# Kernel optimization log

Measured on AMD Instinct MI355X. Metric: run time of the kernel, lower is better.

Reference implementation:

```python
import jax, jax.numpy as jnp
import numpy as np

B, D, H, E = 32768, 128, 512, 16

def setup_inputs() -> dict:
    key = jax.random.key(0)
    ks = jax.random.split(key, 5)
    x = jax.random.normal(ks[0], (B, 1, D), dtype=jnp.float32)
    s1 = 1.0 / float(np.sqrt(H))   # init_ uses last-dim size: w1 last dim = H
    s2 = 1.0 / float(np.sqrt(D))   # w2 last dim = D
    sg = 1.0 / float(np.sqrt(D))   # nn.Linear(D, E) default init scale
    w1 = jax.random.uniform(ks[1], (E, D, H), minval=-s1, maxval=s1, dtype=jnp.float32)
    w2 = jax.random.uniform(ks[2], (E, H, D), minval=-s2, maxval=s2, dtype=jnp.float32)
    wg = jax.random.uniform(ks[3], (D, E), minval=-sg, maxval=sg, dtype=jnp.float32)
    bg = jax.random.uniform(ks[4], (E,), minval=-sg, maxval=sg, dtype=jnp.float32)
    return {"x": x, "w1": w1, "w2": w2, "wg": wg, "bg": bg}

def reference(x, w1, w2, wg, bg):
    xt = x[:, 0, :]                                   # (B, D); seq dim is 1 by construction
    logits = xt @ wg + bg                             # (B, E)
    topk_vals, topk_idx = jax.lax.top_k(logits, 1)    # (B, 1) each
    scores = jax.nn.softmax(topk_vals, axis=-1)       # (B, 1); all ones for k=1
    # every expert processes every token (faithful to the reference)
    hidden = jax.nn.gelu(jnp.einsum('bd,edh->ebh', xt, w1), approximate=False)  # (E, B, H)
    eout = jnp.einsum('ebh,ehd->ebd', hidden, w2)     # (E, B, D)
    # gather selected expert per token, scale, sum over k
    sel = jnp.take_along_axis(eout.transpose(1, 0, 2), topk_idx[:, :, None], axis=1)  # (B, 1, D)
    return (sel * scores[:, :, None]).sum(axis=1)     # (B, D)
```

## Files before the change

### kernel.cpp

```cpp
#include <hip/hip_runtime.h>
#include <hip/hip_bf16.h>
#include <math.h>

#define NB 32768
#define DD 128
#define HH 512
#define EE 16
#define TM 64

typedef __attribute__((ext_vector_type(8))) short short8;
typedef __attribute__((ext_vector_type(4))) float f32x4;
typedef __attribute__((ext_vector_type(16))) float f32x16;

__device__ __forceinline__ unsigned short f2bf(float f) {
  union { float f; unsigned u; } v; v.f = f;
  unsigned r = v.u + 0x7fffu + ((v.u >> 16) & 1u);
  return (unsigned short)(r >> 16);
}

__device__ __forceinline__ float fast_erf(float z) {
  float a = fabsf(z);
  float t = __builtin_amdgcn_rcpf(1.0f + 0.3275911f * a);
  float y = t * (0.254829592f + t * (-0.284496736f + t * (1.421413741f +
            t * (-1.453152027f + t * 1.061405429f))));
  float r = 1.0f - y * __expf(-a * a);
  return z < 0.0f ? -r : r;
}

__global__ __launch_bounds__(256) void prep_kernel(
    const float* __restrict__ x, const float* __restrict__ wg,
    const float* __restrict__ bg, const float* __restrict__ w1,
    const float* __restrict__ w2, int* __restrict__ counts,
    int* __restrict__ rows, unsigned short* __restrict__ wP) {
  __shared__ __align__(16) char smem[50816];
  int tid = threadIdx.x;

  if (blockIdx.x >= 512) {
    int l = tid & 63, lc = l & 31, hi = l >> 5;
    int gw = (blockIdx.x - 512) * 4 + (tid >> 6);
    #pragma unroll
    for (int i = 0; i < 2; ++i) {
      int kb = gw * 2 + i;
      int e = kb >> 8, v = kb & 255;
      float vals[8];
      if (v < 128) {
        int hc = v >> 4, t = (v >> 3) & 1, ks = v & 7;
        int h = hc * 64 + t * 32 + lc;
        const float* src = w1 + (size_t)e * DD * HH + h;
        int d0 = ks * 16 + hi * 8;
        #pragma unroll
        for (int j = 0; j < 8; ++j) vals[j] = src[(size_t)(d0 + j) * HH];
      } else {
        int b2 = v - 128;
        int hc = b2 >> 4, s = (b2 >> 2) & 3, dt = b2 & 3;
        int dout = dt * 32 + lc;
        const float* src = w2 + (size_t)e * HH * DD + dout;
        #pragma unroll
        for (int j = 0; j < 8; ++j) {
          int hp = hc * 64 + (s >> 1) * 32 + (j & 3) + 8 * ((s & 1) + 2 * (j >> 2)) + 4 * hi;
          vals[j] = src[(size_t)hp * DD];
        }
      }
      ushort4 p0, p1;
      p0.x = f2bf(vals[0]); p0.y = f2bf(vals[1]); p0.z = f2bf(vals[2]); p0.w = f2bf(vals[3]);
      p1.x = f2bf(vals[4]); p1.y = f2bf(vals[5]); p1.z = f2bf(vals[6]); p1.w = f2bf(vals[7]);
      unsigned short* dst = wP + (size_t)kb * 512 + l * 8;
      *(ushort4*)dst = p0;
      *(ushort4*)(dst + 4) = p1;
    }
    return;
  }

  float  (*sx)[132] = (float (*)[132])smem;
  double (*swg)[EE] = (double (*)[EE])(smem + 33792);
  int* lcnt  = (int*)(smem + 50176);
  int* gbase = lcnt + EE;
  int* lslot = gbase + EE;
  int* lexp  = lslot + 64;

  int base = blockIdx.x * 64;
  if (tid < EE) lcnt[tid] = 0;
  for (int i = tid; i < DD * EE; i += 256) swg[i >> 4][i & 15] = (double)wg[i];
  {
    int r = tid >> 2, c0 = (tid & 3) * 32;
    const float4* src = (const float4*)(x + (size_t)(base + r) * DD + c0);
    #pragma unroll
    for (int i = 0; i < 8; ++i)
      *(float4*)&sx[r][c0 + i * 4] = src[i];
  }
  __syncthreads();

  int r = tid >> 2;
  int e0 = (tid & 3) * 4;
  double acc[4];
  #pragma unroll
  for (int j = 0; j < 4; ++j) acc[j] = (double)bg[e0 + j];

  #pragma unroll 4
  for (int d = 0; d < DD; ++d) {
    double xv = (double)sx[r][d];
    #pragma unroll
    for (int j = 0; j < 4; ++j)
      acc[j] += xv * swg[d][e0 + j];
  }

  int beste = 0; double bestv = acc[0];
  #pragma unroll
  for (int j = 1; j < 4; ++j)
    if (acc[j] > bestv) { bestv = acc[j]; beste = j; }
  int ge = e0 + beste;

  #pragma unroll
  for (int off = 1; off < 4; off <<= 1) {
    double ov = __shfl_xor(bestv, off);
    int oe = __shfl_xor(ge, off);
    if (ov > bestv || (ov == bestv && oe < ge)) { bestv = ov; ge = oe; }
  }

  if ((tid & 3) == 0) {
    lslot[r] = atomicAdd(&lcnt[ge], 1);
    lexp[r] = ge;
  }
  __syncthreads();
  if (tid < EE && lcnt[tid] > 0)
    gbase[tid] = atomicAdd(&counts[tid], lcnt[tid]);
  __syncthreads();
  if ((tid & 3) == 0) {
    int e2 = lexp[r];
    rows[e2 * NB + gbase[e2] + lslot[r]] = base + r;
  }
}

__global__ __launch_bounds__(128, 2) void moe_gemm(
    const float* __restrict__ x, const unsigned short* __restrict__ wP,
    const int* __restrict__ counts, const int* __restrict__ rows,
    float* __restrict__ out) {
  int e = blockIdx.x;
  int cnt = counts[e];
  int base = blockIdx.y * TM;
  if (base >= cnt) return;

  int tid = threadIdx.x;
  int wv = tid >> 6, l = tid & 63;
  int lc = l & 31, hi = l >> 5;
  int mb = base + wv * 32;
  if (mb >= cnt) return;

  const unsigned short* we = wP + (size_t)e * 256 * 512;

  short8 xa[8];
  {
    int ridx = mb + lc; if (ridx >= cnt) ridx = cnt - 1;
    int grow = rows[e * NB + ridx];
    const float* xr = x + (size_t)grow * DD + hi * 8;
    #pragma unroll
    for (int ks = 0; ks < 8; ++ks) {
      f32x4 v0 = *(const f32x4*)(xr + ks * 16);
      f32x4 v1 = *(const f32x4*)(xr + ks * 16 + 4);
      short8 a;
      a[0] = f2bf(v0[0]); a[1] = f2bf(v0[1]); a[2] = f2bf(v0[2]); a[3] = f2bf(v0[3]);
      a[4] = f2bf(v1[0]); a[5] = f2bf(v1[1]); a[6] = f2bf(v1[2]); a[7] = f2bf(v1[3]);
      xa[ks] = a;
    }
  }

  f32x16 acc2[4];
  #pragma unroll
  for (int dt = 0; dt < 4; ++dt)
    #pragma unroll
    for (int r = 0; r < 16; ++r) acc2[dt][r] = 0.f;

  for (int hc = 0; hc < 8; ++hc) {
    const unsigned short* wc1 = we + (size_t)hc * 16 * 512 + l * 8;
    const unsigned short* wc2 = we + (size_t)(128 + hc * 16) * 512 + l * 8;
    #pragma unroll
    for (int t = 0; t < 2; ++t) {
      f32x16 a1;
      #pragma unroll
      for (int r = 0; r < 16; ++r) a1[r] = 0.f;
      #pragma unroll
      for (int ks = 0; ks < 8; ++ks) {
        short8 wf = *(const short8*)(wc1 + (t * 8 + ks) * 512);
        a1 = __builtin_amdgcn_mfma_f32_32x32x16_bf16(wf, xa[ks], a1, 0, 0, 0);
      }
      #pragma unroll
      for (int s2 = 0; s2 < 2; ++s2) {
        short8 hf8;
        #pragma unroll
        for (int j = 0; j < 8; ++j) {
          int r = (j & 3) | (s2 << 2) | ((j >> 2) << 3);
          float v = a1[r];
          float g = 0.5f * v * (1.0f + fast_erf(v * 0.70710678118654752f));
          hf8[j] = (short)f2bf(g);
        }
        int s = 2 * t + s2;
        #pragma unroll
        for (int dt = 0; dt < 4; ++dt) {
          short8 wf = *(const short8*)(wc2 + (s * 4 + dt) * 512);
          acc2[dt] = __builtin_amdgcn_mfma_f32_32x32x16_bf16(hf8, wf, acc2[dt], 0, 0, 0);
        }
      }
    }
  }

  #pragma unroll
  for (int reg = 0; reg < 16; ++reg) {
    int m = (reg & 3) + 8 * (reg >> 2) + 4 * hi;
    int ridx = mb + m;
    if (ridx < cnt) {
      int grow = rows[e * NB + ridx];
      float* op = out + (size_t)grow * DD + lc;
      op[0]  = acc2[0][reg];
      op[32] = acc2[1][reg];
      op[64] = acc2[2][reg];
      op[96] = acc2[3][reg];
    }
  }
}

extern "C" void kernel_launch(void* const* d_in, const int* in_sizes, int n_in,
                              void* d_out, int out_size, void* d_ws, size_t ws_size,
                              hipStream_t stream) {
  const float* x  = (const float*)d_in[0];
  const float* w1 = (const float*)d_in[1];
  const float* w2 = (const float*)d_in[2];
  const float* wg = (const float*)d_in[3];
  const float* bg = (const float*)d_in[4];
  float* out = (float*)d_out;

  int* counts = (int*)d_ws;
  int* rows   = (int*)((char*)d_ws + 1024);
  unsigned short* wP = (unsigned short*)((char*)d_ws + 1024 + (size_t)EE * NB * 4);

  hipMemsetAsync(d_ws, 0, 64, stream);
  hipLaunchKernelGGL(prep_kernel, dim3(1024), dim3(256), 0, stream,
                     x, wg, bg, w1, w2, counts, rows, wP);
  hipLaunchKernelGGL(moe_gemm, dim3(EE, NB / TM), dim3(128), 0, stream,
                     x, wP, counts, rows, out);
}
```

Before: 139.7 us.

## Split MoE hidden dimension across four waves with shared-memory reduction

Each block of the MoE GEMM now handles 32 token rows with four waves. Each wave covers a quarter of the hidden dimension (two of eight H-chunks) instead of one wave covering all of H for 32 rows. The partial second-GEMM accumulators are reduced through 32 KB of LDS in two tree steps, and the final stores are split across two waves. This shortens the serial per-wave chain and raises parallelism when per-expert token counts are uneven. The cost is extra LDS traffic, three barriers, and 32 KB of shared memory per block, which may limit occupancy.

```diff
diff --git a/kernel.cpp b/kernel.cpp
--- a/kernel.cpp
+++ b/kernel.cpp
@@ -6,7 +6,7 @@
 #define DD 128
 #define HH 512
 #define EE 16
-#define TM 64
+#define TM 32
 
 typedef __attribute__((ext_vector_type(8))) short short8;
 typedef __attribute__((ext_vector_type(4))) float f32x4;
@@ -131,7 +131,7 @@
   }
 }
 
-__global__ __launch_bounds__(128, 2) void moe_gemm(
+__global__ __launch_bounds__(256, 4) void moe_gemm(
     const float* __restrict__ x, const unsigned short* __restrict__ wP,
     const int* __restrict__ counts, const int* __restrict__ rows,
     float* __restrict__ out) {
@@ -140,17 +140,17 @@
   int base = blockIdx.y * TM;
   if (base >= cnt) return;
 
+  __shared__ float sc[8192];
+
   int tid = threadIdx.x;
-  int wv = tid >> 6, l = tid & 63;
+  int hq = tid >> 6, l = tid & 63;
   int lc = l & 31, hi = l >> 5;
-  int mb = base + wv * 32;
-  if (mb >= cnt) return;
 
   const unsigned short* we = wP + (size_t)e * 256 * 512;
 
   short8 xa[8];
   {
-    int ridx = mb + lc; if (ridx >= cnt) ridx = cnt - 1;
+    int ridx = base + lc; if (ridx >= cnt) ridx = cnt - 1;
     int grow = rows[e * NB + ridx];
     const float* xr = x + (size_t)grow * DD + hi * 8;
     #pragma unroll
@@ -170,7 +170,9 @@
     #pragma unroll
     for (int r = 0; r < 16; ++r) acc2[dt][r] = 0.f;
 
-  for (int hc = 0; hc < 8; ++hc) {
+  #pragma unroll
+  for (int hcL = 0; hcL < 2; ++hcL) {
+    int hc = hq * 2 + hcL;
     const unsigned short* wc1 = we + (size_t)hc * 16 * 512 + l * 8;
     const unsigned short* wc2 = we + (size_t)(128 + hc * 16) * 512 + l * 8;
     #pragma unroll
@@ -203,17 +205,52 @@
     }
   }
 
-  #pragma unroll
-  for (int reg = 0; reg < 16; ++reg) {
-    int m = (reg & 3) + 8 * (reg >> 2) + 4 * hi;
-    int ridx = mb + m;
-    if (ridx < cnt) {
-      int grow = rows[e * NB + ridx];
-      float* op = out + (size_t)grow * DD + lc;
-      op[0]  = acc2[0][reg];
-      op[32] = acc2[1][reg];
-      op[64] = acc2[2][reg];
-      op[96] = acc2[3][reg];
+  if (hq & 1) {
+    float* d = sc + (hq >> 1) * 4096;
+    #pragma unroll
+    for (int dt = 0; dt < 4; ++dt)
+      #pragma unroll
+      for (int r = 0; r < 16; ++r) d[(dt * 16 + r) * 64 + l] = acc2[dt][r];
+  }
+  __syncthreads();
+  if (!(hq & 1)) {
+    const float* s = sc + (hq >> 1) * 4096;
+    #pragma unroll
+    for (int dt = 0; dt < 4; ++dt)
+      #pragma unroll
+      for (int r = 0; r < 16; ++r) acc2[dt][r] += s[(dt * 16 + r) * 64 + l];
+  }
+  __syncthreads();
+  if (hq == 0) {
+    #pragma unroll
+    for (int dt = 2; dt < 4; ++dt)
+      #pragma unroll
+      for (int r = 0; r < 16; ++r) sc[((dt - 2) * 16 + r) * 64 + l] = acc2[dt][r];
+  }
+  if (hq == 2) {
+    #pragma unroll
+    for (int dt = 0; dt < 2; ++dt)
+      #pragma unroll
+      for (int r = 0; r < 16; ++r) sc[4096 + (dt * 16 + r) * 64 + l] = acc2[dt][r];
+  }
+  __syncthreads();
+  if (hq == 0 || hq == 2) {
+    int dt0 = (hq == 0) ? 0 : 2;
+    const float* s = (hq == 0) ? (sc + 4096) : sc;
+    #pragma unroll
+    for (int dd2 = 0; dd2 < 2; ++dd2)
+      #pragma unroll
+      for (int r = 0; r < 16; ++r) acc2[dt0 + dd2][r] += s[(dd2 * 16 + r) * 64 + l];
+    #pragma unroll
+    for (int reg = 0; reg < 16; ++reg) {
+      int m = (reg & 3) + 8 * (reg >> 2) + 4 * hi;
+      int ridx = base + m;
+      if (ridx < cnt) {
+        int grow = rows[e * NB + ridx];
+        float* op = out + (size_t)grow * DD + dt0 * 32 + lc;
+        op[0]  = acc2[dt0][reg];
+        op[32] = acc2[dt0 + 1][reg];
+      }
     }
   }
 }
@@ -235,6 +272,6 @@
   hipMemsetAsync(d_ws, 0, 64, stream);
   hipLaunchKernelGGL(prep_kernel, dim3(1024), dim3(256), 0, stream,
                      x, wg, bg, w1, w2, counts, rows, wP);
-  hipLaunchKernelGGL(moe_gemm, dim3(EE, NB / TM), dim3(128), 0, stream,
+  hipLaunchKernelGGL(moe_gemm, dim3(EE, NB / TM), dim3(256), 0, stream,
                      x, wP, counts, rows, out);
 }
```

Measured after the change: 143.9 us. +3.0%, slower.

## Split hidden dim across wave pairs and use persistent grid-stride tiles in MoE GEMM

Applied to the files above, without the earlier changes.

The MoE GEMM now launches a fixed grid of 16x64 blocks with 256 threads. Each block grid-strides over 64-row tiles of its expert instead of launching one block per possible tile, most of which exit early. Within a block, two wave pairs each handle half the hidden dimension for the same rows, and partial outputs are reduced through shared memory before the store. This removes the cost of many empty blocks and doubles parallelism per tile, at the cost of LDS traffic, two barriers per tile, and possible load imbalance across experts.

```diff
diff --git a/kernel.cpp b/kernel.cpp
--- a/kernel.cpp
+++ b/kernel.cpp
@@ -7,6 +7,7 @@
 #define HH 512
 #define EE 16
 #define TM 64
+#define GY 64
 
 typedef __attribute__((ext_vector_type(8))) short short8;
 typedef __attribute__((ext_vector_type(4))) float f32x4;
@@ -131,90 +132,108 @@
   }
 }
 
-__global__ __launch_bounds__(128, 2) void moe_gemm(
+__global__ __launch_bounds__(256, 2) void moe_gemm(
     const float* __restrict__ x, const unsigned short* __restrict__ wP,
     const int* __restrict__ counts, const int* __restrict__ rows,
     float* __restrict__ out) {
   int e = blockIdx.x;
   int cnt = counts[e];
-  int base = blockIdx.y * TM;
-  if (base >= cnt) return;
+
+  __shared__ float sc[8192];
 
   int tid = threadIdx.x;
   int wv = tid >> 6, l = tid & 63;
   int lc = l & 31, hi = l >> 5;
-  int mb = base + wv * 32;
-  if (mb >= cnt) return;
+  int rt = wv & 1;
+  int hh = wv >> 1;
 
   const unsigned short* we = wP + (size_t)e * 256 * 512;
 
-  short8 xa[8];
-  {
-    int ridx = mb + lc; if (ridx >= cnt) ridx = cnt - 1;
-    int grow = rows[e * NB + ridx];
-    const float* xr = x + (size_t)grow * DD + hi * 8;
-    #pragma unroll
-    for (int ks = 0; ks < 8; ++ks) {
-      f32x4 v0 = *(const f32x4*)(xr + ks * 16);
-      f32x4 v1 = *(const f32x4*)(xr + ks * 16 + 4);
-      short8 a;
-      a[0] = f2bf(v0[0]); a[1] = f2bf(v0[1]); a[2] = f2bf(v0[2]); a[3] = f2bf(v0[3]);
-      a[4] = f2bf(v1[0]); a[5] = f2bf(v1[1]); a[6] = f2bf(v1[2]); a[7] = f2bf(v1[3]);
-      xa[ks] = a;
-    }
-  }
-
-  f32x16 acc2[4];
-  #pragma unroll
-  for (int dt = 0; dt < 4; ++dt)
-    #pragma unroll
-    for (int r = 0; r < 16; ++r) acc2[dt][r] = 0.f;
-
-  for (int hc = 0; hc < 8; ++hc) {
-    const unsigned short* wc1 = we + (size_t)hc * 16 * 512 + l * 8;
-    const unsigned short* wc2 = we + (size_t)(128 + hc * 16) * 512 + l * 8;
-    #pragma unroll
-    for (int t = 0; t < 2; ++t) {
-      f32x16 a1;
-      #pragma unroll
-      for (int r = 0; r < 16; ++r) a1[r] = 0.f;
+  for (int ty = blockIdx.y; ty * TM < cnt; ty += GY) {
+    int mb = ty * TM + rt * 32;
+
+    short8 xa[8];
+    {
+      int ridx = mb + lc; if (ridx >= cnt) ridx = cnt - 1;
+      int grow = rows[e * NB + ridx];
+      const float* xr = x + (size_t)grow * DD + hi * 8;
       #pragma unroll
       for (int ks = 0; ks < 8; ++ks) {
-        short8 wf = *(const short8*)(wc1 + (t * 8 + ks) * 512);
-        a1 = __builtin_amdgcn_mfma_f32_32x32x16_bf16(wf, xa[ks], a1, 0, 0, 0);
-      }
-      #pragma unroll
-      for (int s2 = 0; s2 < 2; ++s2) {
-        short8 hf8;
-        #pragma unroll
-        for (int j = 0; j < 8; ++j) {
-          int r = (j & 3) | (s2 << 2) | ((j >> 2) << 3);
-          float v = a1[r];
-          float g = 0.5f * v * (1.0f + fast_erf(v * 0.70710678118654752f));
-          hf8[j] = (short)f2bf(g);
-        }
-        int s = 2 * t + s2;
-        #pragma unroll
-        for (int dt = 0; dt < 4; ++dt) {
-          short8 wf = *(const short8*)(wc2 + (s * 4 + dt) * 512);
-          acc2[dt] = __builtin_amdgcn_mfma_f32_32x32x16_bf16(hf8, wf, acc2[dt], 0, 0, 0);
-        }
-      }
-    }
-  }
-
-  #pragma unroll
-  for (int reg = 0; reg < 16; ++reg) {
-    int m = (reg & 3) + 8 * (reg >> 2) + 4 * hi;
-    int ridx = mb + m;
-    if (ridx < cnt) {
-      int grow = rows[e * NB + ridx];
-      float* op = out + (size_t)grow * DD + lc;
-      op[0]  = acc2[0][reg];
-      op[32] = acc2[1][reg];
-      op[64] = acc2[2][reg];
-      op[96] = acc2[3][reg];
-    }
+        f32x4 v0 = *(const f32x4*)(xr + ks * 16);
+        f32x4 v1 = *(const f32x4*)(xr + ks * 16 + 4);
+        short8 a;
+        a[0] = f2bf(v0[0]); a[1] = f2bf(v0[1]); a[2] = f2bf(v0[2]); a[3] = f2bf(v0[3]);
+        a[4] = f2bf(v1[0]); a[5] = f2bf(v1[1]); a[6] = f2bf(v1[2]); a[7] = f2bf(v1[3]);
+        xa[ks] = a;
+      }
+    }
+
+    f32x16 acc2[4];
+    #pragma unroll
+    for (int dt = 0; dt < 4; ++dt)
+      #pragma unroll
+      for (int r = 0; r < 16; ++r) acc2[dt][r] = 0.f;
+
+    #pragma unroll
+    for (int hcL = 0; hcL < 4; ++hcL) {
+      int hc = hh * 4 + hcL;
+      const unsigned short* wc1 = we + (size_t)hc * 16 * 512 + l * 8;
+      const unsigned short* wc2 = we + (size_t)(128 + hc * 16) * 512 + l * 8;
+      #pragma unroll
+      for (int t = 0; t < 2; ++t) {
+        f32x16 a1;
+        #pragma unroll
+        for (int r = 0; r < 16; ++r) a1[r] = 0.f;
+        #pragma unroll
+        for (int ks = 0; ks < 8; ++ks) {
+          short8 wf = *(const short8*)(wc1 + (t * 8 + ks) * 512);
+          a1 = __builtin_amdgcn_mfma_f32_32x32x16_bf16(wf, xa[ks], a1, 0, 0, 0);
+        }
+        #pragma unroll
+        for (int s2 = 0; s2 < 2; ++s2) {
+          short8 hf8;
+          #pragma unroll
+          for (int j = 0; j < 8; ++j) {
+            int r = (j & 3) | (s2 << 2) | ((j >> 2) << 3);
+            float v = a1[r];
+            float g = 0.5f * v * (1.0f + fast_erf(v * 0.70710678118654752f));
+            hf8[j] = (short)f2bf(g);
+          }
+          int s = 2 * t + s2;
+          #pragma unroll
+          for (int dt = 0; dt < 4; ++dt) {
+            short8 wf = *(const short8*)(wc2 + (s * 4 + dt) * 512);
+            acc2[dt] = __builtin_amdgcn_mfma_f32_32x32x16_bf16(hf8, wf, acc2[dt], 0, 0, 0);
+          }
+        }
+      }
+    }
+
+    if (hh == 1) {
+      float* d = sc + rt * 4096;
+      #pragma unroll
+      for (int dt = 0; dt < 4; ++dt)
+        #pragma unroll
+        for (int r = 0; r < 16; ++r) d[(dt * 16 + r) * 64 + l] = acc2[dt][r];
+    }
+    __syncthreads();
+    if (hh == 0) {
+      const float* s = sc + rt * 4096;
+      #pragma unroll
+      for (int reg = 0; reg < 16; ++reg) {
+        int m = (reg & 3) + 8 * (reg >> 2) + 4 * hi;
+        int ridx = mb + m;
+        if (ridx < cnt) {
+          int grow = rows[e * NB + ridx];
+          float* op = out + (size_t)grow * DD + lc;
+          op[0]  = acc2[0][reg] + s[(0 * 16 + reg) * 64 + l];
+          op[32] = acc2[1][reg] + s[(1 * 16 + reg) * 64 + l];
+          op[64] = acc2[2][reg] + s[(2 * 16 + reg) * 64 + l];
+          op[96] = acc2[3][reg] + s[(3 * 16 + reg) * 64 + l];
+        }
+      }
+    }
+    __syncthreads();
   }
 }
 
@@ -235,6 +254,6 @@
   hipMemsetAsync(d_ws, 0, 64, stream);
   hipLaunchKernelGGL(prep_kernel, dim3(1024), dim3(256), 0, stream,
                      x, wg, bg, w1, w2, counts, rows, wP);
-  hipLaunchKernelGGL(moe_gemm, dim3(EE, NB / TM), dim3(128), 0, stream,
+  hipLaunchKernelGGL(moe_gemm, dim3(EE, GY), dim3(256), 0, stream,
                      x, wP, counts, rows, out);
 }
```

Measured after the change: 235.1 us. +68.3%, slower.
